# Optimization experiments

Hardware: AMD Instinct MI355X
Metric: run time of the kernel (lower is better)

## Reference

```python
import jax, jax.numpy as jnp
import numpy as np

B, M, F_IN, DX, K, L, N_ALL = 8192, 10, 128, 128, 64, 32, 100000
NN = M - 1          # n_neigh
INF = float(M)


def layer_norm(x, g, b, eps=1e-5):
    mu = x.mean(-1, keepdims=True)
    var = ((x - mu) ** 2).mean(-1, keepdims=True)
    return (x - mu) * jax.lax.rsqrt(var + eps) * g + b


def bfs_dists(adj, mask):
    # normalized all-pairs hop distances via repeated boolean matmul (m=10 fixed)
    adj_bin = (adj > 1e-5).astype(jnp.float32)
    eye = jnp.eye(M, dtype=bool)
    d = jnp.where(eye[None], 0.0, jnp.where(adj_bin > 0, 1.0, INF))
    curr = adj_bin
    for k in range(2, M):
        curr = jnp.matmul(curr, adj_bin)
        d = jnp.where((curr > 0) & (d == INF), float(k), d)
    mask2 = mask[:, :, None] * mask[:, None, :]
    d = jnp.where(mask2 == 0, INF, d)
    return d / float(M)


def compute_sw(zb, zp, theta, vmask):
    # sliced Wasserstein-2 between batch point clouds [B,NN,d] and prototypes [K,NN,d]
    tn = theta / jnp.linalg.norm(theta, axis=1, keepdims=True)
    pb = jnp.einsum('bmd,ld->bml', zb, tn)
    pp = jnp.einsum('kmd,ld->kml', zp, tn)
    idx = jnp.argsort(pb, axis=1)
    pbs = jnp.take_along_axis(pb, idx, axis=1)
    pps = jnp.sort(pp, axis=1)
    w = jnp.take_along_axis(jnp.broadcast_to(vmask[:, :, None], pb.shape), idx, axis=1)
    w = w / (w.sum(axis=1, keepdims=True) + 1e-9)
    # sum_m w*(pb-pp)^2 expanded to avoid materializing [B,K,NN,L]
    t1 = (w * pbs ** 2).sum(axis=1)                   # [B,L]
    t2 = jnp.einsum('bml,kml->bkl', w * pbs, pps)     # [B,K,L]
    t3 = jnp.einsum('bml,kml->bkl', w, pps ** 2)
    return (t1[:, None, :] - 2.0 * t2 + t3).mean(axis=-1)


def compute_radial(rb, rp, vmask):
    idx = jnp.argsort(rb, axis=1)
    rbs = jnp.take_along_axis(rb, idx, axis=1)
    rps = jnp.sort(rp, axis=1)
    w = jnp.take_along_axis(vmask, idx, axis=1)
    w = w / (w.sum(axis=1, keepdims=True) + 1e-9)
    return (((rbs[:, None, :] - rps[None]) ** 2) * w[:, None, :]).sum(-1)


def setup_inputs() -> dict:
    key = jax.random.key(0)
    ks = jax.random.split(key, 16)
    up = (jax.random.uniform(ks[0], (B, M, M)) < 0.3).astype(jnp.float32)
    adj = jnp.maximum(up, up.transpose(0, 2, 1)) * (1.0 - jnp.eye(M))
    features = jax.random.normal(ks[1], (N_ALL, F_IN), jnp.float32)
    idxs = jax.random.randint(ks[2], (B, M), 0, N_ALL + 1)   # N_ALL == padding index
    rn = lambda k, s, sc=0.02: sc * jax.random.normal(k, s, jnp.float32)
    params = dict(
        x_lin_w=rn(ks[3], (F_IN, DX), 0.05), x_lin_b=jnp.zeros((DX,)),
        x_ln_g=jnp.ones((DX,)), x_ln_b=jnp.zeros((DX,)),
        s_ln_g=jnp.ones((NN,)), s_ln_b=jnp.zeros((NN,)),
        theta_x=jax.random.normal(ks[4], (L, DX), jnp.float32),
        theta_s=jax.random.normal(ks[5], (L, NN), jnp.float32),
        alpha_raw=jnp.zeros(()),
        an_w1=rn(ks[6], (DX, 32), 0.1), an_b1=jnp.zeros((32,)),
        an_w2=rn(ks[7], (32, 1), 0.1), an_b2=jnp.zeros((1,)),
        wn_w1=rn(ks[8], (2 * DX, 32), 0.1), wn_b1=jnp.zeros((32,)),
        wn_w2=rn(ks[9], (32, 1), 0.1), wn_b2=jnp.zeros((1,)),
        w_raw=jnp.zeros(()),
        proto_root=jax.random.normal(ks[10], (K, F_IN), jnp.float32),
        proto_neigh=jax.random.normal(ks[11], (K, NN, F_IN), jnp.float32),
        proto_rad=jax.random.uniform(ks[12], (K, NN)),
        proto_dn=jax.random.uniform(ks[13], (NN * (NN - 1) // 2, K), minval=-0.5, maxval=0.5),
        log_gamma=jnp.asarray(np.log(0.01), jnp.float32),
    )
    return {"adj": adj, "features": features, "idxs": idxs, **params}


def reference(adj, features, idxs, x_lin_w, x_lin_b, x_ln_g, x_ln_b, s_ln_g, s_ln_b,
              theta_x, theta_s, alpha_raw, an_w1, an_b1, an_w2, an_b2,
              wn_w1, wn_b1, wn_w2, wn_b2, w_raw,
              proto_root, proto_neigh, proto_rad, proto_dn, log_gamma):
    b = adj.shape[0]
    x_all = jnp.concatenate([features, jnp.zeros((1, F_IN), features.dtype)], 0)
    x_patch = x_all[idxs]                             # [B,M,F]
    x_root, x_neigh = x_patch[:, 0], x_patch[:, 1:]
    vmask = (idxs[:, 1:] != N_ALL).astype(jnp.float32)   # [B,NN]
    lin = lambda x: x @ x_lin_w + x_lin_b
    h_root = layer_norm(lin(x_root), x_ln_g, x_ln_b)
    h_proto_root = layer_norm(lin(proto_root), x_ln_g, x_ln_b)
    d_root_feat = (jnp.sum(h_root ** 2, -1)[:, None] + jnp.sum(h_proto_root ** 2, -1)[None]
                   - 2.0 * h_root @ h_proto_root.T)   # squared cdist [B,K]
    full_mask = jnp.concatenate([jnp.ones((b, 1), jnp.float32), vmask], 1)
    dists_full = bfs_dists(adj, full_mask)
    d_radial_str = compute_radial(dists_full[:, 0, 1:], proto_rad, vmask)
    h_neigh = layer_norm(lin(x_neigh), x_ln_g, x_ln_b)     # dropout = identity (eval)
    h_proto_neigh = layer_norm(lin(proto_neigh), x_ln_g, x_ln_b)
    sw_neigh_feat = compute_sw(h_neigh, h_proto_neigh, theta_x, vmask)
    hs_neigh = layer_norm(jnp.sort(dists_full[:, 1:, 1:], axis=1), s_ln_g, s_ln_b)
    ti, tj = np.triu_indices(NN, 1)
    C = jnp.zeros((K, NN, NN)).at[:, ti, tj].set(jax.nn.sigmoid(proto_dn).T)
    C = C + C.transpose(0, 2, 1)
    hs_proto = layer_norm(jnp.sort(C, axis=1), s_ln_g, s_ln_b)
    sw_neigh_str = compute_sw(hs_neigh, hs_proto, theta_s, vmask)
    h_pooled = (h_neigh * vmask[:, :, None]).sum(1) / (vmask.sum(1, keepdims=True) + 1e-9)
    alpha_logit = jnp.maximum(h_pooled @ an_w1 + an_b1, 0.0) @ an_w2 + an_b2   # [B,1]
    alpha = jax.nn.sigmoid(alpha_raw + alpha_logit)
    # pairwise w_net([h_root; h_proto_root]) without materializing [B,K,2*DX]
    hb = h_root @ wn_w1[:DX] + wn_b1                   # [B,32]
    hp = h_proto_root @ wn_w1[DX:]                     # [K,32]
    w_logit = (jnp.maximum(hb[:, None] + hp[None], 0.0) @ wn_w2)[..., 0] + wn_b2[0]
    w = jax.nn.sigmoid(w_raw + w_logit)                # [B,K]
    d_feat = w * d_root_feat + (1.0 - w) * sw_neigh_feat
    d_str = w * d_radial_str + (1.0 - w) * sw_neigh_str
    d_fgw = alpha * d_feat + (1.0 - alpha) * d_str
    return jnp.exp(-jnp.exp(log_gamma) * d_fgw)        # [B,K]
```

## Files before the change

kernel.cpp:

```cpp
#include <hip/hip_runtime.h>
#include <hip/hip_bf16.h>

typedef unsigned short u16;
typedef __attribute__((ext_vector_type(8))) short short8;
typedef __attribute__((ext_vector_type(4))) float f32x4;

#define NN 9
#define DX 128
#define KP 64
#define LL 32
#define NALL 100000
#define BMAX 8192
#define NBM 16
#define NBP 64
#define HXR 136
#define WSTR 4736

#define MFMA(a, b, c) __builtin_amdgcn_mfma_f32_16x16x32_bf16(a, b, c, 0, 0, 0)
#define WFENCE() __threadfence_block()

__device__ __align__(16) float g_tns[LL * NN];
__device__ __align__(16) float g_hprn[KP];
__device__ __align__(16) float g_hpt[32 * KP];
__device__ __align__(16) float g_rpst[NN * KP];
__device__ __align__(16) u16   g_hroot[BMAX * DX];
__device__ __align__(16) u16   g_hpool[BMAX * DX];
__device__ __align__(16) float g_hrn[BMAX];
__device__ __align__(16) u16   g_Cf[BMAX * 576];
__device__ __align__(16) u16   g_Cs[BMAX * 576];
__device__ __align__(16) float g_drad[BMAX * 64];
__device__ __align__(16) float g_t1x[BMAX];
__device__ __align__(16) float g_t1s[BMAX];
__device__ __align__(16) u16   g_pW[16384];
__device__ __align__(16) u16   g_pBt[4096];
__device__ __align__(16) u16   g_pBr[8192];
__device__ __align__(16) u16   g_pBx[36864];
__device__ __align__(16) u16   g_pBs[36864];
__device__ __align__(16) u16   g_pAn[4096];
__device__ __align__(16) u16   g_pWn[4096];

__device__ __forceinline__ float bf2f(u16 u) {
    union { unsigned u; float f; } v; v.u = ((unsigned)u) << 16; return v.f;
}
__device__ __forceinline__ u16 f2bf(float f) {
    __hip_bfloat16 h = __float2bfloat16(f);
    union { __hip_bfloat16 h; u16 u; } v; v.h = h; return v.u;
}
__device__ __forceinline__ float ldv(const void* p, long i, int f32) {
    return f32 ? ((const float*)p)[i] : bf2f(((const u16*)p)[i]);
}
__device__ __forceinline__ float sigmoidf(float x) { return 1.f / (1.f + expf(-x)); }

__device__ __forceinline__ int bfrag_idx(int ksteps, int ncol, int kd) {
    int ntile = ncol >> 4, n = ncol & 15;
    int kstep = kd >> 5, quad = (kd >> 3) & 3, j = kd & 7;
    return ((ntile * ksteps + kstep) * 64 + quad * 16 + n) * 8 + j;
}

__device__ __forceinline__ void rank9(const float* v, int* r) {
#pragma unroll
    for (int m = 0; m < 9; m++) {
        int rk = 0;
#pragma unroll
        for (int n = 0; n < 9; n++)
            rk += (v[n] < v[m]) || (v[n] == v[m] && n < m);
        r[m] = rk;
    }
}

__global__ __launch_bounds__(256) void k_pack(
    const void* xlw, const void* theta_x, const void* theta_s,
    const void* an_w1, const void* wn_w1, const void* proto_rad, const void* xlg) {
    int t = threadIdx.x;
    const int f32 = (((const u16*)xlg)[0] == 0);
    if (blockIdx.x == 0) {
        for (int i = t; i < 16384; i += 256) {
            int c = i >> 7, d = i & 127;
            g_pW[bfrag_idx(4, d, c)] = f2bf(ldv(xlw, i, f32));
        }
    } else if (blockIdx.x == 1) {
        if (t < 32) {
            float s = 0;
            for (int d = 0; d < 128; d++) { float v = ldv(theta_x, t * 128 + d, f32); s = fmaf(v, v, s); }
            float inv = 1.f / sqrtf(s);
            for (int d = 0; d < 128; d++)
                g_pBt[bfrag_idx(4, t, d)] = f2bf(ldv(theta_x, t * 128 + d, f32) * inv);
        } else if (t < 64) {
            int l = t - 32;
            float s = 0;
            for (int j = 0; j < 9; j++) { float v = ldv(theta_s, l * 9 + j, f32); s = fmaf(v, v, s); }
            float inv = 1.f / sqrtf(s);
            for (int j = 0; j < 9; j++) g_tns[l * 9 + j] = ldv(theta_s, l * 9 + j, f32) * inv;
        } else if (t < 128) {
            int k = t - 64;
            float v[9]; int r[9];
#pragma unroll
            for (int m = 0; m < 9; m++) v[m] = ldv(proto_rad, k * 9 + m, f32);
            rank9(v, r);
#pragma unroll
            for (int m = 0; m < 9; m++) g_rpst[r[m] * 64 + k] = v[m];
        }
    } else {
        for (int i = t; i < 4096; i += 256) {
            int d = i >> 5, j = i & 31;
            g_pAn[bfrag_idx(4, j, d)] = f2bf(ldv(an_w1, i, f32));
            g_pWn[bfrag_idx(4, j, d)] = f2bf(ldv(wn_w1, i, f32));
        }
    }
}

__global__ __launch_bounds__(256, 5) void k_lin(
    const void* adj, const void* feat, const int* idxs,
    const void* proto_root, const void* proto_neigh,
    const void* xlb, const void* xlg, const void* xlbt,
    const void* slg, const void* slb, const void* wn_w1,
    const void* proto_dn, int B) {
    __shared__ __align__(16) char sm[4 * WSTR];

    int t = threadIdx.x, lane = t & 63, w = t >> 6;
    const int f32 = (((const u16*)xlg)[0] == 0);
    int fm = lane & 15, quad = lane >> 4;
    bool isProto = (blockIdx.x < (unsigned)NBP);

    if (!isProto) {
        u16*   hSw = (u16*)(sm + w * WSTR);
        float* pbw = (float*)(sm + w * WSTR + 2720);
        float* dfw = (float*)(sm + w * WSTR + 3872);
        float* stw = (float*)(sm + w * WSTR + 4272);
        float* rbw = (float*)(sm + w * WSTR + 4608);
        float* wrw = (float*)(sm + w * WSTR + 4644);

        int bw = (blockIdx.x - NBP) * 4 + w;
        if (bw >= B) return;

        bool valid = false;
        if (lane < 10) {
            int id = idxs[bw * 10 + lane];
            valid = (lane == 0) || (id != NALL);
        }
        unsigned long long mb = __ballot(valid);
        float inv = 1.f / ((float)__popcll(mb & 0x3FEull) + 1e-9f);

        bool azero = true; long aoff = 0;
        if (fm < 10) {
            int id2 = idxs[bw * 10 + fm];
            if (id2 != NALL) { azero = false; aoff = (long)id2 * 128; }
        }
        short8 af[4];
#pragma unroll
        for (int ks = 0; ks < 4; ks++) af[ks] = (short8){0, 0, 0, 0, 0, 0, 0, 0};
        if (!azero) {
            if (f32) {
#pragma unroll
                for (int ks = 0; ks < 4; ks++) {
                    const f32x4* src = (const f32x4*)((const float*)feat + aoff + ks * 32 + quad * 8);
                    f32x4 v0 = src[0], v1 = src[1];
                    u16* ap = (u16*)&af[ks];
#pragma unroll
                    for (int j = 0; j < 4; j++) { ap[j] = f2bf(v0[j]); ap[4 + j] = f2bf(v1[j]); }
                }
            } else {
#pragma unroll
                for (int ks = 0; ks < 4; ks++)
                    af[ks] = *(const short8*)((const u16*)feat + aoff + ks * 32 + quad * 8);
            }
        }

        unsigned rowbits = 0;
        if (lane < 10) {
            for (int j = 0; j < 10; j++)
                if (ldv(adj, (long)bw * 100 + lane * 10 + j, f32) > 1e-5f) rowbits |= 1u << j;
        }
        int dl[10];
#pragma unroll
        for (int j = 0; j < 10; j++) dl[j] = (j == lane) ? 0 : (((rowbits >> j) & 1) ? 1 : 10);
        unsigned reach = (lane < 10) ? (rowbits | (1u << lane)) : 0u;
        for (int s = 2; s <= 9; s++) {
            unsigned nr = reach;
#pragma unroll
            for (int j = 0; j < 10; j++) {
                unsigned rj = __shfl(rowbits, j);
                if ((reach >> j) & 1) nr |= rj;
            }
            unsigned add = nr & ~reach;
#pragma unroll
            for (int j = 0; j < 10; j++) if ((add >> j) & 1) dl[j] = s;
            reach = nr;
            if (__all(add == 0)) break;
        }
        if (lane < 10) {
            int mi = (int)((mb >> lane) & 1);
#pragma unroll
            for (int j = 0; j < 10; j++) {
                int mj = (int)((mb >> j) & 1);
                dfw[lane * 10 + j] = (mi && mj) ? (float)dl[j] * 0.1f : 1.0f;
            }
        }
        {
            float v[9];
#pragma unroll
            for (int m = 0; m < 9; m++) {
                float vm = ((mb >> (1 + m)) & 1) ? (float)dl[1 + m] * 0.1f : 1.0f;
                v[m] = __shfl(vm, 0);
            }
            if (lane < 9) {
                float mine = v[0];
#pragma unroll
                for (int m = 1; m < 9; m++) if (lane == m) mine = v[m];
                int rk = 0;
#pragma unroll
                for (int n = 0; n < 9; n++) rk += (v[n] < mine) || (v[n] == mine && n < lane);
                rbw[rk] = mine;
                wrw[rk] = (((mb >> (1 + lane)) & 1) ? 1.f : 0.f) * inv;
            }
        }

        {
            float bias8[8], gg8[8], bb8[8];
#pragma unroll
            for (int nt = 0; nt < 8; nt++) {
                int col = nt * 16 + fm;
                bias8[nt] = ldv(xlb, col, f32);
                gg8[nt]   = ldv(xlg, col, f32);
                bb8[nt]   = ldv(xlbt, col, f32);
            }
            f32x4 acc[8];
#pragma unroll
            for (int nt = 0; nt < 8; nt++) acc[nt] = (f32x4){0.f, 0.f, 0.f, 0.f};
#pragma unroll
            for (int ks = 0; ks < 4; ks++) {
#pragma unroll
                for (int nt = 0; nt < 8; nt++) {
                    short8 bf = *(const short8*)(g_pW + ((nt * 4 + ks) * 64 + lane) * 8);
                    acc[nt] = MFMA(af[ks], bf, acc[nt]);
                }
            }
#pragma unroll
            for (int reg = 0; reg < 4; reg++) {
                float s = 0, q = 0;
#pragma unroll
                for (int nt = 0; nt < 8; nt++) {
                    float v = acc[nt][reg] + bias8[nt];
                    s += v; q = fmaf(v, v, q);
                }
#pragma unroll
                for (int m = 1; m < 16; m <<= 1) { s += __shfl_xor(s, m); q += __shfl_xor(q, m); }
                float mu = s * (1.f / 128.f);
                float var = fmaxf(q * (1.f / 128.f) - mu * mu, 0.f);
                float rs = rsqrtf(var + 1e-5f);
                int rowD = quad * 4 + reg;
                if (rowD < 10) {
#pragma unroll
                    for (int nt = 0; nt < 8; nt++) {
                        float val = (acc[nt][reg] + bias8[nt] - mu) * rs * gg8[nt] + bb8[nt];
                        hSw[rowD * HXR + nt * 16 + fm] = f2bf(val);
                    }
                }
            }
        }
        WFENCE();

        if (lane < 16)
            ((short8*)(g_hroot + (long)bw * 128))[lane] = ((const short8*)hSw)[lane];
        {
            float v0 = bf2f(hSw[lane]), v1 = bf2f(hSw[64 + lane]);
            float q = v0 * v0 + v1 * v1;
#pragma unroll
            for (int m = 32; m >= 1; m >>= 1) q += __shfl_xor(q, m);
            if (lane == 0) g_hrn[bw] = q;
        }
        {
            float a0 = 0, a1 = 0;
            int c0 = lane * 2, c1 = lane * 2 + 1;
#pragma unroll
            for (int m = 0; m < 9; m++) {
                float msk = ((mb >> (1 + m)) & 1) ? 1.f : 0.f;
                a0 = fmaf(bf2f(hSw[(1 + m) * HXR + c0]), msk, a0);
                a1 = fmaf(bf2f(hSw[(1 + m) * HXR + c1]), msk, a1);
            }
            unsigned pk = (unsigned)f2bf(a0 * inv) | ((unsigned)f2bf(a1 * inv) << 16);
            ((unsigned*)(g_hpool + (long)bw * 128))[lane] = pk;
        }

        {
            f32x4 acc0 = {0.f, 0.f, 0.f, 0.f}, acc1 = {0.f, 0.f, 0.f, 0.f};
            const u16* arow = hSw + (1 + fm) * HXR;
#pragma unroll
            for (int ks = 0; ks < 4; ks++) {
                short8 afn = {0, 0, 0, 0, 0, 0, 0, 0};
                if (fm < 9) afn = *(const short8*)(arow + ks * 32 + quad * 8);
                short8 b0 = *(const short8*)(g_pBt + ((0 * 4 + ks) * 64 + lane) * 8);
                short8 b1 = *(const short8*)(g_pBt + ((1 * 4 + ks) * 64 + lane) * 8);
                acc0 = MFMA(afn, b0, acc0);
                acc1 = MFMA(afn, b1, acc1);
            }
#pragma unroll
            for (int reg = 0; reg < 4; reg++) {
                int row = quad * 4 + reg;
                if (row < 9) {
                    pbw[row * 32 + fm]      = acc0[reg];
                    pbw[row * 32 + 16 + fm] = acc1[reg];
                }
            }
        }
        WFENCE();

        {
            float t1 = 0;
            if (lane < 32) {
                float v[9]; int r[9];
#pragma unroll
                for (int m = 0; m < 9; m++) v[m] = pbw[m * 32 + lane];
                rank9(v, r);
#pragma unroll
                for (int m = 0; m < 9; m++) {
                    float wgt = (((mb >> (1 + m)) & 1) ? 1.f : 0.f) * inv;
                    int slot = lane * 9 + r[m];
                    g_Cf[(long)bw * 576 + slot]       = f2bf(wgt);
                    g_Cf[(long)bw * 576 + 288 + slot] = f2bf(-2.f * wgt * v[m]);
                    t1 = fmaf(wgt * v[m], v[m], t1);
                }
            }
#pragma unroll
            for (int m = 16; m >= 1; m >>= 1) t1 += __shfl_xor(t1, m);
            if (lane == 0) g_t1x[bw] = t1;
        }
        if (lane < 9) {
            float v[9]; int r[9];
#pragma unroll
            for (int i = 0; i < 9; i++) v[i] = dfw[(1 + i) * 10 + 1 + lane];
            rank9(v, r);
#pragma unroll
            for (int i = 0; i < 9; i++) stw[r[i] * 9 + lane] = v[i];
        }
        WFENCE();
        if (lane < 9) {
            float vv[9];
#pragma unroll
            for (int j = 0; j < 9; j++) vv[j] = stw[lane * 9 + j];
            float mu = 0;
#pragma unroll
            for (int j = 0; j < 9; j++) mu += vv[j];
            mu *= (1.f / 9.f);
            float var = 0;
#pragma unroll
            for (int j = 0; j < 9; j++) { float d0 = vv[j] - mu; var = fmaf(d0, d0, var); }
            var *= (1.f / 9.f);
            float rs = rsqrtf(var + 1e-5f);
#pragma unroll
            for (int j = 0; j < 9; j++)
                stw[lane * 9 + j] = (vv[j] - mu) * rs * ldv(slg, j, f32) + ldv(slb, j, f32);
        }
        WFENCE();
        {
            int l = lane & 31;
            int m0 = (lane < 32) ? 0 : 5, m1 = (lane < 32) ? 5 : 9;
            for (int m = m0; m < m1; m++) {
                float a = 0;
#pragma unroll
                for (int j = 0; j < 9; j++) a = fmaf(stw[m * 9 + j], g_tns[l * 9 + j], a);
                pbw[m * 32 + l] = a;
            }
        }
        WFENCE();
        {
            float t1 = 0;
            if (lane < 32) {
                float v[9]; int r[9];
#pragma unroll
                for (int m = 0; m < 9; m++) v[m] = pbw[m * 32 + lane];
                rank9(v, r);
#pragma unroll
                for (int m = 0; m < 9; m++) {
                    float wgt = (((mb >> (1 + m)) & 1) ? 1.f : 0.f) * inv;
                    int slot = lane * 9 + r[m];
                    g_Cs[(long)bw * 576 + slot]       = f2bf(wgt);
                    g_Cs[(long)bw * 576 + 288 + slot] = f2bf(-2.f * wgt * v[m]);
                    t1 = fmaf(wgt * v[m], v[m], t1);
                }
            }
#pragma unroll
            for (int m = 16; m >= 1; m >>= 1) t1 += __shfl_xor(t1, m);
            if (lane == 0) g_t1s[bw] = t1;
        }
        {
            float a = 0;
#pragma unroll
            for (int m = 0; m < 9; m++) {
                float d0 = rbw[m] - g_rpst[m * 64 + lane];
                a = fmaf(d0 * d0, wrw[m], a);
            }
            g_drad[(long)bw * 64 + lane] = a;
        }
        return;
    }

    u16*   hXpb = (u16*)sm;
    float* pbX  = (float*)(sm + 2560);
    float* Cm   = (float*)(sm + 3712);
    float* hsnP = (float*)(sm + 4048);
    int kb = blockIdx.x;

    if (w == 0) {
        const void* abuf; long aoff;
        if (fm < 9) { abuf = proto_neigh; aoff = (long)(kb * 9 + fm) * 128; }
        else        { abuf = proto_root;  aoff = (long)kb * 128; }
        bool arow = (fm < 10);
        short8 af[4];
#pragma unroll
        for (int ks = 0; ks < 4; ks++) af[ks] = (short8){0, 0, 0, 0, 0, 0, 0, 0};
        if (arow) {
            if (f32) {
#pragma unroll
                for (int ks = 0; ks < 4; ks++) {
                    const f32x4* src = (const f32x4*)((const float*)abuf + aoff + ks * 32 + quad * 8);
                    f32x4 v0 = src[0], v1 = src[1];
                    u16* ap = (u16*)&af[ks];
#pragma unroll
                    for (int j = 0; j < 4; j++) { ap[j] = f2bf(v0[j]); ap[4 + j] = f2bf(v1[j]); }
                }
            } else {
#pragma unroll
                for (int ks = 0; ks < 4; ks++)
                    af[ks] = *(const short8*)((const u16*)abuf + aoff + ks * 32 + quad * 8);
            }
        }
        float bias8[8], gg8[8], bb8[8];
#pragma unroll
        for (int nt = 0; nt < 8; nt++) {
            int col = nt * 16 + fm;
            bias8[nt] = ldv(xlb, col, f32);
            gg8[nt]   = ldv(xlg, col, f32);
            bb8[nt]   = ldv(xlbt, col, f32);
        }
        f32x4 acc[8];
#pragma unroll
        for (int nt = 0; nt < 8; nt++) acc[nt] = (f32x4){0.f, 0.f, 0.f, 0.f};
#pragma unroll
        for (int ks = 0; ks < 4; ks++) {
#pragma unroll
            for (int nt = 0; nt < 8; nt++) {
                short8 bf = *(const short8*)(g_pW + ((nt * 4 + ks) * 64 + lane) * 8);
                acc[nt] = MFMA(af[ks], bf, acc[nt]);
            }
        }
#pragma unroll
        for (int reg = 0; reg < 4; reg++) {
            float s = 0, q = 0;
#pragma unroll
            for (int nt = 0; nt < 8; nt++) {
                float v = acc[nt][reg] + bias8[nt];
                s += v; q = fmaf(v, v, q);
            }
#pragma unroll
            for (int m = 1; m < 16; m <<= 1) { s += __shfl_xor(s, m); q += __shfl_xor(q, m); }
            float mu = s * (1.f / 128.f);
            float var = fmaxf(q * (1.f / 128.f) - mu * mu, 0.f);
            float rs = rsqrtf(var + 1e-5f);
            int rowD = quad * 4 + reg;
            if (rowD < 10) {
#pragma unroll
                for (int nt = 0; nt < 8; nt++) {
                    float val = (acc[nt][reg] + bias8[nt] - mu) * rs * gg8[nt] + bb8[nt];
                    hXpb[rowD * 128 + nt * 16 + fm] = f2bf(val);
                }
            }
        }
    }
    __syncthreads();

    for (int i = t; i < 128; i += 256)
        g_pBr[bfrag_idx(4, kb, i)] = hXpb[1152 + i];
    if (w == 0) {
        float v0 = bf2f(hXpb[1152 + lane]);
        float v1 = bf2f(hXpb[1216 + lane]);
        float q = v0 * v0 + v1 * v1;
#pragma unroll
        for (int m = 32; m >= 1; m >>= 1) q += __shfl_xor(q, m);
        if (lane == 0) g_hprn[kb] = q;
    }
    {
        int j = t >> 3, sub = t & 7;
        float a = 0;
#pragma unroll
        for (int dd = 0; dd < 16; dd++) {
            int d = sub * 16 + dd;
            a = fmaf(bf2f(hXpb[1152 + d]), ldv(wn_w1, (128 + d) * 32 + j, f32), a);
        }
        a += __shfl_xor(a, 1);
        a += __shfl_xor(a, 2);
        a += __shfl_xor(a, 4);
        if (sub == 0) g_hpt[j * 64 + kb] = a;
    }
    if (w == 0) {
        f32x4 acc0 = {0.f, 0.f, 0.f, 0.f}, acc1 = {0.f, 0.f, 0.f, 0.f};
        const u16* arow2 = hXpb + fm * 128;
#pragma unroll
        for (int ks = 0; ks < 4; ks++) {
            short8 afp = {0, 0, 0, 0, 0, 0, 0, 0};
            if (fm < 9) afp = *(const short8*)(arow2 + ks * 32 + quad * 8);
            short8 b0 = *(const short8*)(g_pBt + ((0 * 4 + ks) * 64 + lane) * 8);
            short8 b1 = *(const short8*)(g_pBt + ((1 * 4 + ks) * 64 + lane) * 8);
            acc0 = MFMA(afp, b0, acc0);
            acc1 = MFMA(afp, b1, acc1);
        }
#pragma unroll
        for (int reg = 0; reg < 4; reg++) {
            int row = quad * 4 + reg;
            if (row < 9) {
                pbX[row * 32 + fm]      = acc0[reg];
                pbX[row * 32 + 16 + fm] = acc1[reg];
            }
        }
    }
    for (int i = t; i < 81; i += 256) {
        int ii = i / 9, jj = i % 9; float v = 0.f;
        if (ii != jj) {
            int a = (ii < jj) ? ii : jj, b2 = (ii < jj) ? jj : ii;
            int p = a * 8 - a * (a - 1) / 2 + (b2 - a - 1);
            v = sigmoidf(ldv(proto_dn, p * 64 + kb, f32));
        }
        Cm[i] = v;
    }
    __syncthreads();
    if (t < 32) {
        float v[9]; int r[9];
#pragma unroll
        for (int m = 0; m < 9; m++) v[m] = pbX[m * 32 + t];
        rank9(v, r);
#pragma unroll
        for (int m = 0; m < 9; m++) {
            int kd = t * 9 + r[m];
            g_pBx[bfrag_idx(18, kb, kd)]       = f2bf(v[m] * v[m]);
            g_pBx[bfrag_idx(18, kb, 288 + kd)] = f2bf(v[m]);
        }
    }
    if (t >= 64 && t < 73) {
        int col = t - 64;
        float v[9]; int r[9];
#pragma unroll
        for (int j = 0; j < 9; j++) v[j] = Cm[j * 9 + col];
        rank9(v, r);
#pragma unroll
        for (int j = 0; j < 9; j++) Cm[r[j] * 9 + col] = v[j];
    }
    __syncthreads();
    if (t < 9) {
        float mu = 0;
#pragma unroll
        for (int j = 0; j < 9; j++) mu += Cm[t * 9 + j];
        mu *= (1.f / 9.f);
        float var = 0;
#pragma unroll
        for (int j = 0; j < 9; j++) { float d0 = Cm[t * 9 + j] - mu; var = fmaf(d0, d0, var); }
        var *= (1.f / 9.f);
        float rs = rsqrtf(var + 1e-5f);
#pragma unroll
        for (int j = 0; j < 9; j++)
            hsnP[t * 9 + j] = (Cm[t * 9 + j] - mu) * rs * ldv(slg, j, f32) + ldv(slb, j, f32);
    }
    __syncthreads();
    if (t < 32) {
#pragma unroll
        for (int m = 0; m < 9; m++) {
            float a = 0;
#pragma unroll
            for (int j = 0; j < 9; j++) a = fmaf(hsnP[m * 9 + j], g_tns[t * 9 + j], a);
            pbX[m * 32 + t] = a;
        }
    }
    __syncthreads();
    if (t < 32) {
        float v[9]; int r[9];
#pragma unroll
        for (int m = 0; m < 9; m++) v[m] = pbX[m * 32 + t];
        rank9(v, r);
#pragma unroll
        for (int m = 0; m < 9; m++) {
            int kd = t * 9 + r[m];
            g_pBs[bfrag_idx(18, kb, kd)]       = f2bf(v[m] * v[m]);
            g_pBs[bfrag_idx(18, kb, 288 + kd)] = f2bf(v[m]);
        }
    }
}

struct M3 {
    u16   Cf[NBM][584];
    u16   Cs[NBM][584];
    u16   hrootL[NBM][136];
    u16   hpoolb[NBM][136];
    float drad[NBM][65];
    float hbv[NBM][33];
    float sc[NBM][9];
};
__global__ __launch_bounds__(1024, 8) void k_main(
    const void* an_b1, const void* an_w2, const void* an_b2,
    const void* wn_b1, const void* wn_w2, const void* wn_b2,
    const void* alpha_raw, const void* w_raw, const void* log_gamma,
    const void* xlg, void* out, int B) {
    __shared__ __align__(16) M3 S;
    int t = threadIdx.x, lane = t & 63, w = t >> 6;
    const int f32 = (((const u16*)xlg)[0] == 0);
    int fm = lane & 15, quad = lane >> 4;
    int bw = blockIdx.x * NBM + w;
    bool bv = (bw < B);

    if (bv) {
        {
            const short8* src = (const short8*)(g_Cf + (long)bw * 576);
            short8* dst = (short8*)S.Cf[w];
            for (int i = lane; i < 72; i += 64) dst[i] = src[i];
        }
        {
            const short8* src = (const short8*)(g_Cs + (long)bw * 576);
            short8* dst = (short8*)S.Cs[w];
            for (int i = lane; i < 72; i += 64) dst[i] = src[i];
        }
        if (lane < 16) {
            ((short8*)S.hrootL[w])[lane] = ((const short8*)(g_hroot + (long)bw * 128))[lane];
            ((short8*)S.hpoolb[w])[lane] = ((const short8*)(g_hpool + (long)bw * 128))[lane];
        }
        S.drad[w][lane] = g_drad[(long)bw * 64 + lane];
        if (lane == 0) {
            S.sc[w][1] = g_hrn[bw];
            S.sc[w][3] = g_t1x[bw];
            S.sc[w][4] = g_t1s[bw];
        }
    } else {
        short8 z = {0, 0, 0, 0, 0, 0, 0, 0};
        for (int i = lane; i < 72; i += 64) {
            ((short8*)S.Cf[w])[i] = z;
            ((short8*)S.Cs[w])[i] = z;
        }
        if (lane < 16) {
            ((short8*)S.hrootL[w])[lane] = z;
            ((short8*)S.hpoolb[w])[lane] = z;
        }
    }
    __syncthreads();

    f32x4 rd = {0.f, 0.f, 0.f, 0.f};
    f32x4 accF = {0.f, 0.f, 0.f, 0.f}, accS = {0.f, 0.f, 0.f, 0.f};
    if (w < 4) {
#pragma unroll
        for (int ks = 0; ks < 4; ks++) {
            short8 af = *(const short8*)(S.hrootL[fm] + ks * 32 + quad * 8);
            short8 bfr = *(const short8*)(g_pBr + ((w * 4 + ks) * 64 + lane) * 8);
            rd = MFMA(af, bfr, rd);
        }
#pragma unroll
        for (int ks = 0; ks < 18; ks++) {
            short8 aF = *(const short8*)(S.Cf[fm] + ks * 32 + quad * 8);
            short8 aS = *(const short8*)(S.Cs[fm] + ks * 32 + quad * 8);
            short8 bF = *(const short8*)(g_pBx + ((w * 18 + ks) * 64 + lane) * 8);
            short8 bS = *(const short8*)(g_pBs + ((w * 18 + ks) * 64 + lane) * 8);
            accF = MFMA(aF, bF, accF);
            accS = MFMA(aS, bS, accS);
        }
    } else if (w == 4) {
        f32x4 a0 = {0.f, 0.f, 0.f, 0.f}, a1 = {0.f, 0.f, 0.f, 0.f};
#pragma unroll
        for (int ks = 0; ks < 4; ks++) {
            short8 af = *(const short8*)(S.hrootL[fm] + ks * 32 + quad * 8);
            short8 b0 = *(const short8*)(g_pWn + ((0 * 4 + ks) * 64 + lane) * 8);
            short8 b1 = *(const short8*)(g_pWn + ((1 * 4 + ks) * 64 + lane) * 8);
            a0 = MFMA(af, b0, a0);
            a1 = MFMA(af, b1, a1);
        }
        float wb0 = ldv(wn_b1, fm, f32), wb1 = ldv(wn_b1, 16 + fm, f32);
#pragma unroll
        for (int reg = 0; reg < 4; reg++) {
            int b = quad * 4 + reg;
            S.hbv[b][fm]      = a0[reg] + wb0;
            S.hbv[b][16 + fm] = a1[reg] + wb1;
        }
    } else if (w == 5) {
        f32x4 a0 = {0.f, 0.f, 0.f, 0.f}, a1 = {0.f, 0.f, 0.f, 0.f};
#pragma unroll
        for (int ks = 0; ks < 4; ks++) {
            short8 af = *(const short8*)(S.hpoolb[fm] + ks * 32 + quad * 8);
            short8 b0 = *(const short8*)(g_pAn + ((0 * 4 + ks) * 64 + lane) * 8);
            short8 b1 = *(const short8*)(g_pAn + ((1 * 4 + ks) * 64 + lane) * 8);
            a0 = MFMA(af, b0, a0);
            a1 = MFMA(af, b1, a1);
        }
        float ab0 = ldv(an_b1, fm, f32), ab1 = ldv(an_b1, 16 + fm, f32);
        float aw0 = ldv(an_w2, fm, f32), aw1 = ldv(an_w2, 16 + fm, f32);
        float araw = ldv(alpha_raw, 0, f32), ab2 = ldv(an_b2, 0, f32);
#pragma unroll
        for (int reg = 0; reg < 4; reg++) {
            float s = fmaxf(a0[reg] + ab0, 0.f) * aw0 + fmaxf(a1[reg] + ab1, 0.f) * aw1;
            s += __shfl_xor(s, 1); s += __shfl_xor(s, 2);
            s += __shfl_xor(s, 4); s += __shfl_xor(s, 8);
            if (fm == 0) S.sc[quad * 4 + reg][2] = sigmoidf(araw + s + ab2);
        }
    }
    __syncthreads();

    if (w < 4) {
        int k = w * 16 + fm;
        float wb2 = ldv(wn_b2, 0, f32);
        float wr  = ldv(w_raw, 0, f32);
        float gamma = expf(ldv(log_gamma, 0, f32));
        float hprnk = g_hprn[k];
        float wl[4] = {0.f, 0.f, 0.f, 0.f};
#pragma unroll 4
        for (int j = 0; j < 32; j++) {
            float hptv = g_hpt[j * 64 + k];
            float w2v = ldv(wn_w2, j, f32);
#pragma unroll
            for (int reg = 0; reg < 4; reg++)
                wl[reg] = fmaf(fmaxf(S.hbv[quad * 4 + reg][j] + hptv, 0.f), w2v, wl[reg]);
        }
#pragma unroll
        for (int reg = 0; reg < 4; reg++) {
            int b = quad * 4 + reg, bb = blockIdx.x * NBM + b;
            if (bb >= B) continue;
            float swf = (S.sc[b][3] + accF[reg]) * (1.f / 32.f);
            float sws = (S.sc[b][4] + accS[reg]) * (1.f / 32.f);
            float drfk = S.sc[b][1] + hprnk - 2.f * rd[reg];
            float wgt = sigmoidf(wr + wl[reg] + wb2);
            float dfeat = wgt * drfk + (1.f - wgt) * swf;
            float dstr  = wgt * S.drad[b][k] + (1.f - wgt) * sws;
            float al = S.sc[b][2];
            float dfgw = al * dfeat + (1.f - al) * dstr;
            if (!(dfgw == dfgw)) dfgw = 1e30f;
            float res = expf(-gamma * dfgw);
            if (f32) ((float*)out)[(long)bb * 64 + k] = res;
            else     ((u16*)out)[(long)bb * 64 + k] = f2bf(res);
        }
    }
}

extern "C" void kernel_launch(void* const* d_in, const int* in_sizes, int n_in,
                              void* d_out, int out_size, void* d_ws, size_t ws_size,
                              hipStream_t stream) {
    const void* adj  = d_in[0];
    const void* feat = d_in[1];
    const int*  idxs = (const int*)d_in[2];
    const void* xlw  = d_in[3];
    const void* xlb  = d_in[4];
    const void* xlg  = d_in[5];
    const void* xlbt = d_in[6];
    const void* slg  = d_in[7];
    const void* slb  = d_in[8];
    const void* thx  = d_in[9];
    const void* ths  = d_in[10];
    const void* araw = d_in[11];
    const void* anw1 = d_in[12];
    const void* anb1 = d_in[13];
    const void* anw2 = d_in[14];
    const void* anb2 = d_in[15];
    const void* wnw1 = d_in[16];
    const void* wnb1 = d_in[17];
    const void* wnw2 = d_in[18];
    const void* wnb2 = d_in[19];
    const void* wraw = d_in[20];
    const void* prt  = d_in[21];
    const void* prn  = d_in[22];
    const void* prad = d_in[23];
    const void* pdn  = d_in[24];
    const void* lgam = d_in[25];
    int B = in_sizes[2] / 10;
    int NBW = (B + 3) / 4;

    k_pack<<<3, 256, 0, stream>>>(xlw, thx, ths, anw1, wnw1, prad, xlg);
    k_lin<<<NBP + NBW, 256, 0, stream>>>(adj, feat, idxs, prt, prn,
                                         xlb, xlg, xlbt, slg, slb, wnw1,
                                         pdn, B);
    k_main<<<(B + NBM - 1) / NBM, 1024, 0, stream>>>(
                                  anb1, anw2, anb2, wnb1, wnw2, wnb2,
                                  araw, wraw, lgam, xlg, d_out, B);
}
```

Before: 215.0 us.

## Repack LN params, vectorize adj loads, and shuffle projections instead of LDS

The per-wave bias, gamma and beta vectors and the structure LN params are packed once in k_pack into a contiguous float buffer. k_lin preloads them into registers and distributes them with shuffles instead of doing scattered ldv reads. Adjacency rows are now loaded with vectorized float2/uint loads, and the two projection results (pbw) are redistributed with cross-lane shuffles instead of a shared-memory round trip plus fences. This shrinks per-wave LDS, and it adds shuffle work and register pressure.

```diff
diff --git a/kernel.cpp b/kernel.cpp
--- a/kernel.cpp
+++ b/kernel.cpp
@@ -14,7 +14,7 @@
 #define NBM 16
 #define NBP 64
 #define HXR 136
-#define WSTR 4736
+#define WSTR 3584
 
 #define MFMA(a, b, c) __builtin_amdgcn_mfma_f32_16x16x32_bf16(a, b, c, 0, 0, 0)
 #define WFENCE() __threadfence_block()
@@ -23,6 +23,7 @@
 __device__ __align__(16) float g_hprn[KP];
 __device__ __align__(16) float g_hpt[32 * KP];
 __device__ __align__(16) float g_rpst[NN * KP];
+__device__ __align__(16) float g_prm[416];
 __device__ __align__(16) u16   g_hroot[BMAX * DX];
 __device__ __align__(16) u16   g_hpool[BMAX * DX];
 __device__ __align__(16) float g_hrn[BMAX];
@@ -70,7 +71,9 @@
 
 __global__ __launch_bounds__(256) void k_pack(
     const void* xlw, const void* theta_x, const void* theta_s,
-    const void* an_w1, const void* wn_w1, const void* proto_rad, const void* xlg) {
+    const void* an_w1, const void* wn_w1, const void* proto_rad,
+    const void* xlb, const void* xlg, const void* xlbt,
+    const void* slg, const void* slb) {
     int t = threadIdx.x;
     const int f32 = (((const u16*)xlg)[0] == 0);
     if (blockIdx.x == 0) {
@@ -106,6 +109,15 @@
             g_pAn[bfrag_idx(4, j, d)] = f2bf(ldv(an_w1, i, f32));
             g_pWn[bfrag_idx(4, j, d)] = f2bf(ldv(wn_w1, i, f32));
         }
+        for (int i = t; i < 402; i += 256) {
+            float v;
+            if (i < 128)      v = ldv(xlb,  i,       f32);
+            else if (i < 256) v = ldv(xlg,  i - 128, f32);
+            else if (i < 384) v = ldv(xlbt, i - 256, f32);
+            else if (i < 393) v = ldv(slg,  i - 384, f32);
+            else              v = ldv(slb,  i - 393, f32);
+            g_prm[i] = v;
+        }
     }
 }
 
@@ -124,14 +136,17 @@
 
     if (!isProto) {
         u16*   hSw = (u16*)(sm + w * WSTR);
-        float* pbw = (float*)(sm + w * WSTR + 2720);
-        float* dfw = (float*)(sm + w * WSTR + 3872);
-        float* stw = (float*)(sm + w * WSTR + 4272);
-        float* rbw = (float*)(sm + w * WSTR + 4608);
-        float* wrw = (float*)(sm + w * WSTR + 4644);
+        float* dfw = (float*)(sm + w * WSTR + 2720);
+        float* stw = (float*)(sm + w * WSTR + 3120);
+        float* rbw = (float*)(sm + w * WSTR + 3456);
+        float* wrw = (float*)(sm + w * WSTR + 3496);
 
         int bw = (blockIdx.x - NBP) * 4 + w;
         if (bw >= B) return;
+
+        float r0 = g_prm[lane],       r1 = g_prm[64 + lane];
+        float r2 = g_prm[128 + lane], r3 = g_prm[192 + lane];
+        float r4 = g_prm[256 + lane], r5 = g_prm[320 + lane];
 
         bool valid = false;
         if (lane < 10) {
@@ -168,8 +183,23 @@
 
         unsigned rowbits = 0;
         if (lane < 10) {
+            float ev[10];
+            if (f32) {
+#pragma unroll
+                for (int k = 0; k < 5; k++) {
+                    float2 p = ((const float2*)adj)[(long)bw * 50 + lane * 5 + k];
+                    ev[2 * k] = p.x; ev[2 * k + 1] = p.y;
+                }
+            } else {
+#pragma unroll
+                for (int k = 0; k < 5; k++) {
+                    unsigned p = ((const unsigned*)adj)[(long)bw * 50 + lane * 5 + k];
+                    ev[2 * k] = bf2f((u16)p); ev[2 * k + 1] = bf2f((u16)(p >> 16));
+                }
+            }
+#pragma unroll
             for (int j = 0; j < 10; j++)
-                if (ldv(adj, (long)bw * 100 + lane * 10 + j, f32) > 1e-5f) rowbits |= 1u << j;
+                if (ev[j] > 1e-5f) rowbits |= 1u << j;
         }
         int dl[10];
 #pragma unroll
@@ -219,10 +249,10 @@
             float bias8[8], gg8[8], bb8[8];
 #pragma unroll
             for (int nt = 0; nt < 8; nt++) {
-                int col = nt * 16 + fm;
-                bias8[nt] = ldv(xlb, col, f32);
-                gg8[nt]   = ldv(xlg, col, f32);
-                bb8[nt]   = ldv(xlbt, col, f32);
+                int src = (nt * 16 + fm) & 63;
+                bias8[nt] = __shfl(nt < 4 ? r0 : r1, src);
+                gg8[nt]   = __shfl(nt < 4 ? r2 : r3, src);
+                bb8[nt]   = __shfl(nt < 4 ? r4 : r5, src);
             }
             f32x4 acc[8];
 #pragma unroll
@@ -294,23 +324,17 @@
                 acc0 = MFMA(afn, b0, acc0);
                 acc1 = MFMA(afn, b1, acc1);
             }
-#pragma unroll
-            for (int reg = 0; reg < 4; reg++) {
-                int row = quad * 4 + reg;
-                if (row < 9) {
-                    pbw[row * 32 + fm]      = acc0[reg];
-                    pbw[row * 32 + 16 + fm] = acc1[reg];
-                }
-            }
-        }
-        WFENCE();
-
-        {
+            float v[9];
+#pragma unroll
+            for (int m = 0; m < 9; m++) {
+                int src = (m >> 2) * 16 + (lane & 15);
+                float s0 = __shfl(acc0[m & 3], src);
+                float s1 = __shfl(acc1[m & 3], src);
+                v[m] = ((lane & 31) < 16) ? s0 : s1;
+            }
             float t1 = 0;
             if (lane < 32) {
-                float v[9]; int r[9];
-#pragma unroll
-                for (int m = 0; m < 9; m++) v[m] = pbw[m * 32 + lane];
+                int r[9];
                 rank9(v, r);
 #pragma unroll
                 for (int m = 0; m < 9; m++) {
@@ -325,6 +349,7 @@
             for (int m = 16; m >= 1; m >>= 1) t1 += __shfl_xor(t1, m);
             if (lane == 0) g_t1x[bw] = t1;
         }
+
         if (lane < 9) {
             float v[9]; int r[9];
 #pragma unroll
@@ -349,26 +374,30 @@
             float rs = rsqrtf(var + 1e-5f);
 #pragma unroll
             for (int j = 0; j < 9; j++)
-                stw[lane * 9 + j] = (vv[j] - mu) * rs * ldv(slg, j, f32) + ldv(slb, j, f32);
+                stw[lane * 9 + j] = (vv[j] - mu) * rs * g_prm[384 + j] + g_prm[393 + j];
         }
         WFENCE();
         {
             int l = lane & 31;
-            int m0 = (lane < 32) ? 0 : 5, m1 = (lane < 32) ? 5 : 9;
-            for (int m = m0; m < m1; m++) {
+            float pa[5];
+#pragma unroll
+            for (int mm = 0; mm < 5; mm++) {
+                int m = (lane < 32) ? mm : mm + 5;
                 float a = 0;
-#pragma unroll
-                for (int j = 0; j < 9; j++) a = fmaf(stw[m * 9 + j], g_tns[l * 9 + j], a);
-                pbw[m * 32 + l] = a;
-            }
-        }
-        WFENCE();
-        {
+                if (m < 9) {
+#pragma unroll
+                    for (int j = 0; j < 9; j++) a = fmaf(stw[m * 9 + j], g_tns[l * 9 + j], a);
+                }
+                pa[mm] = a;
+            }
+            float v[9];
+#pragma unroll
+            for (int m = 0; m < 5; m++) v[m] = pa[m];
+#pragma unroll
+            for (int m = 5; m < 9; m++) v[m] = __shfl(pa[m - 5], (lane & 31) + 32);
             float t1 = 0;
             if (lane < 32) {
-                float v[9]; int r[9];
-#pragma unroll
-                for (int m = 0; m < 9; m++) v[m] = pbw[m * 32 + lane];
+                int r[9];
                 rank9(v, r);
 #pragma unroll
                 for (int m = 0; m < 9; m++) {
@@ -764,7 +793,8 @@
     int B = in_sizes[2] / 10;
     int NBW = (B + 3) / 4;
 
-    k_pack<<<3, 256, 0, stream>>>(xlw, thx, ths, anw1, wnw1, prad, xlg);
+    k_pack<<<3, 256, 0, stream>>>(xlw, thx, ths, anw1, wnw1, prad,
+                                  xlb, xlg, xlbt, slg, slb);
     k_lin<<<NBP + NBW, 256, 0, stream>>>(adj, feat, idxs, prt, prn,
                                          xlb, xlg, xlbt, slg, slb, wnw1,
                                          pdn, B);
```

New measurement: 218.4 us. No clear change (+1.6%).
